# Optimization experiments

Measured on AMD Instinct MI355X. Metric: run time of the kernel, lower is better.

The kernel has to match this reference:

```python
import jax, jax.numpy as jnp
import numpy as np

R, B, F, C, NCLS = 32, 4096, 256, 4, 1000  # n_rules, batch, n_fea, n_channel, n_cls
K, PAD, POOL = 5, 1, 2                     # kernel_size, padding, pooling_size


def setup_inputs() -> dict:
    key = jax.random.key(0)
    ks = jax.random.split(key, 12)
    L0 = F + 2 * PAD - K + 1          # 254 after conv1
    L1 = L0 // POOL                   # 127 after avgpool1
    L2 = (L1 + 2 * PAD - K + 1) // POOL  # 62 after conv2+avgpool2
    att = C * L2                      # 248 (matches torch att_size formula)
    hid = att // 2                    # 124
    s = lambda k, shape: jax.random.normal(k, shape, dtype=jnp.float32) * 0.05
    return dict(
        data=jax.random.normal(ks[0], (B, F), dtype=jnp.float32),
        proto=s(ks[1], (R, F)),
        conv1_w=s(ks[2], (C, 1, K)), conv1_b=s(ks[3], (C,)),
        conv2_w=s(ks[4], (C, C, K)), conv2_b=s(ks[5], (C,)),
        fc1_w=s(ks[6], (att, hid)), fc1_b=s(ks[7], (hid,)),
        fc2_w=s(ks[8], (hid, 1)), fc2_b=s(ks[9], (1,)),
        consq_w=s(ks[10], (R, F, NCLS)), consq_b=s(ks[11], (R, NCLS)),
        is_train=0,
    )


def _conv1d(x, w, b):
    # x: [N, Cin, L], w: [Cout, Cin, K]
    out = jax.lax.conv_general_dilated(
        x, w, window_strides=(1,), padding=[(PAD, PAD)],
        dimension_numbers=('NCH', 'OIH', 'NCH'))
    return out + b[None, :, None]


def _avgpool2(x):
    # non-overlapping AvgPool1d(2), drops trailing remainder like torch
    L2 = x.shape[-1] // POOL
    return x[..., :L2 * POOL].reshape(x.shape[0], x.shape[1], L2, POOL).mean(-1)


def reference(data, proto, conv1_w, conv1_b, conv2_w, conv2_b,
              fc1_w, fc1_b, fc2_w, fc2_b, consq_w, consq_b, is_train):
    n_batch = data.shape[0]
    # data_diff: [R, B, F] -> shared gating net, fold rules into batch
    diff = (data[None, :, :] - proto[:, None, :]).reshape(R * n_batch, 1, F)
    h = _avgpool2(jax.nn.relu(_conv1d(diff, conv1_w, conv1_b)))
    h = _avgpool2(jax.nn.relu(_conv1d(h, conv2_w, conv2_b)))
    h = h.reshape(R * n_batch, -1)                       # [R*B, att]
    h = jax.nn.relu(h @ fc1_w + fc1_b)                   # [R*B, hid]
    fs_ini = jnp.tanh(h @ fc2_w + fc2_b)                 # [R*B, 1]
    fs_ini = fs_ini.reshape(R, n_batch).T                # cat(dim=1) -> [B, R]
    fs = jax.nn.softmax(fs_ini, axis=1)                  # softmax over rules
    # per-rule experts: grouped matmul [B,F] x [R,F,NCLS]
    expert = jnp.einsum('bf,rfc->rbc', data, consq_w) + consq_b[:, None, :]
    return jnp.einsum('br,rbc->bc', fs, expert)          # [B, NCLS]
```

## Files before the change

kernel.cpp:

```cpp
#include <hip/hip_runtime.h>
#include <hip/hip_bf16.h>

using bf16x8 = __attribute__((ext_vector_type(8))) short;
using f32x4  = __attribute__((ext_vector_type(4))) float;
using v2f    = __attribute__((ext_vector_type(2))) float;

__device__ __forceinline__ unsigned short f2bf_rne(float x) {
    unsigned u = __float_as_uint(x);
    u += 0x7fffu + ((u >> 16) & 1u);
    return (unsigned short)(u >> 16);
}

__device__ __forceinline__ float sload(float v) {
    return __uint_as_float(__builtin_amdgcn_readfirstlane(__float_as_uint(v)));
}

__device__ __forceinline__ void gload_lds16(const void* g, void* l) {
    __builtin_amdgcn_global_load_lds(
        (const __attribute__((address_space(1))) unsigned int*)g,
        (__attribute__((address_space(3))) unsigned int*)l, 16, 0, 0);
}

constexpr int KP = 8320;
constexpr int KROW = KP * 2;

constexpr size_t OFF_DT  = 0;
constexpr size_t OFF_Q1  = OFF_DT  + (size_t)260 * 4096 * 4;
constexpr size_t OFF_BT  = OFF_Q1  + (size_t)32 * 1024 * 4;
constexpr size_t OFF_C1P = OFF_BT;
constexpr size_t OFF_W1S = OFF_BT  + (size_t)1024 * KP * 2;
constexpr size_t OFF_FSI = OFF_W1S + (size_t)128 * 256 * 2;
constexpr size_t OFF_FS  = OFF_FSI + (size_t)32 * 4096 * 4;
constexpr size_t OFF_ASC = OFF_FS  + (size_t)32 * 4096 * 4;
constexpr size_t OFF_H2  = OFF_ASC;
constexpr size_t OFF_P1  = OFF_ASC + (size_t)4096 * KP * 2;

__global__ __launch_bounds__(256) void k_transpose(const float* __restrict__ data,
                                                   float* __restrict__ dTp) {
    __shared__ float tile[64][65];
    int bx = blockIdx.x & 63;
    int fx = blockIdx.x >> 6;
    int tx = threadIdx.x & 63, ty4 = threadIdx.x >> 6;
#pragma unroll
    for (int i = 0; i < 16; ++i) {
        int ty = ty4 * 16 + i;
        tile[ty][tx] = data[(bx * 64 + ty) * 256 + fx * 64 + tx];
    }
    __syncthreads();
#pragma unroll
    for (int i = 0; i < 16; ++i) {
        int ty = ty4 * 16 + i;
        dTp[(size_t)(fx * 64 + ty + 1) * 4096 + bx * 64 + tx] = tile[tx][ty];
    }
}

__global__ __launch_bounds__(256) void k_zrows(float* __restrict__ dTp) {
    int i = blockIdx.x * 256 + threadIdx.x;
    dTp[i] = 0.f;
    dTp[(size_t)257 * 4096 + i] = 0.f;
}

__global__ __launch_bounds__(256) void k_prep_proto(const float* __restrict__ proto,
                                                    const float* __restrict__ w1,
                                                    const float* __restrict__ b1,
                                                    float* __restrict__ q1p) {
    __shared__ float ps[256];
    __shared__ float w1s[20];
    int r = blockIdx.x, tid = threadIdx.x;
    ps[tid] = proto[r * 256 + tid];
    if (tid < 20) w1s[tid] = w1[tid];
    __syncthreads();
    if (tid < 254) {
#pragma unroll
        for (int c = 0; c < 4; ++c) {
            float s = -b1[c];
#pragma unroll
            for (int k = 0; k < 5; ++k) {
                int x = tid + k - 1;
                float xv = (x >= 0 && x < 256) ? ps[x] : 0.f;
                s += w1s[c * 5 + k] * xv;
            }
            q1p[r * 1024 + c * 256 + tid] = s;
        }
    }
}

__global__ __launch_bounds__(64) void k_prep_c1d(const float* __restrict__ dTp,
                                                 const float* __restrict__ w1,
                                                 float2* __restrict__ c1p) {
    int lane = threadIdx.x;
    int bg = blockIdx.x >> 3, ch = blockIdx.x & 7;
    int l0 = ch << 4;
    int nl = (ch == 7) ? 15 : 16;
    int b = (bg << 6) + lane;
    float w1r[20];
#pragma unroll
    for (int i = 0; i < 20; ++i) w1r[i] = w1[i];
    const float* dp = dTp + (size_t)(2 * l0) * 4096 + b;
    float d[6];
#pragma unroll
    for (int i = 0; i < 6; ++i) d[i] = dp[(size_t)i * 4096];
    dp += (size_t)6 * 4096;
    float2* outp = c1p + b;
    for (int li = 0; li < nl; ++li) {
        int l = l0 + li;
#pragma unroll
        for (int c = 0; c < 4; ++c) {
            float s0 = 0.f, s1 = 0.f;
#pragma unroll
            for (int k = 0; k < 5; ++k) {
                s0 += w1r[c * 5 + k] * d[k];
                s1 += w1r[c * 5 + k] * d[k + 1];
            }
            outp[(size_t)(c * 127 + l) * 4096] = make_float2(s0, s1);
        }
        d[0] = d[2]; d[1] = d[3]; d[2] = d[4]; d[3] = d[5];
        d[4] = dp[0];
        d[5] = dp[4096];
        dp += 8192;
    }
}

__global__ __launch_bounds__(256) void k_castB(const float* __restrict__ cw,
                                               const float* __restrict__ cb,
                                               unsigned short* __restrict__ BT) {
    __shared__ unsigned short L[64 * 137];
    int tid = threadIdx.x;
    int kt = blockIdx.x >> 3, ct = blockIdx.x & 7;
    int k0 = kt << 6, c0 = ct << 7;
#pragma unroll
    for (int i = 0; i < 32; ++i) {
        int flat = i * 256 + tid;
        int cl = flat & 127, kl = flat >> 7;
        int cg = c0 + cl;
        int kg = k0 + kl;
        float v = 0.f;
        if (cg < 1000) {
            if (kg < 8192) v = cw[(size_t)kg * 1000 + cg];
            else if (kg < 8224) v = cb[(size_t)(kg - 8192) * 1000 + cg];
        }
        L[kl * 137 + cl] = f2bf_rne(v);
    }
    __syncthreads();
#pragma unroll
    for (int i = 0; i < 4; ++i) {
        int task = i * 256 + tid;
        int kg = task & 7, cl = task >> 3;
        int base = kg * 8 * 137 + cl;
        unsigned x = (unsigned)L[base] | ((unsigned)L[base + 137] << 16);
        unsigned y = (unsigned)L[base + 2 * 137] | ((unsigned)L[base + 3 * 137] << 16);
        unsigned z = (unsigned)L[base + 4 * 137] | ((unsigned)L[base + 5 * 137] << 16);
        unsigned w = (unsigned)L[base + 6 * 137] | ((unsigned)L[base + 7 * 137] << 16);
        uint4 o; o.x = x; o.y = y; o.z = z; o.w = w;
        int cg = c0 + cl;
        size_t byte = (size_t)cg * KROW + (size_t)(kt << 7) + (size_t)((kg ^ (cg & 7)) << 4);
        *(uint4*)((char*)BT + byte) = o;
    }
}

__global__ __launch_bounds__(256) void k_castW(const float* __restrict__ fc1w,
                                               unsigned short* __restrict__ W1s) {
    int idx = blockIdx.x * 256 + threadIdx.x;
    int col = idx >> 8, k = idx & 255;
    float v = 0.f;
    if (col < 124 && k < 248) {
        int f = (k & 3) * 62 + (k >> 2);
        v = fc1w[f * 124 + col];
    }
    int byte = col * 512 + ((k >> 6) << 7) + ((((k >> 3) & 7) ^ (col & 7)) << 4) + ((k & 7) << 1);
    *(unsigned short*)((char*)W1s + byte) = f2bf_rne(v);
}

__global__ __attribute__((amdgpu_waves_per_eu(3, 4))) __launch_bounds__(64)
void k_conv2(const float2* __restrict__ c1p,
             const float* __restrict__ q1p,
             const float* __restrict__ w2,
             const float* __restrict__ b2,
             char* __restrict__ h2c) {
    __shared__ unsigned short T[64 * 72];

    int lane = threadIdx.x;
    int job = blockIdx.x;
    int jh = job & 1;
    int bc = (job >> 1) & 63;
    int r  = job >> 7;
    int b0 = bc << 6;
    int b = b0 + lane;
    int rb0 = r * 4096 + b0;
    int j2s = jh ? 32 : 0;
    int j2e = jh ? 62 : 32;

    float w2r[80];
#pragma unroll
    for (int i = 0; i < 80; ++i) w2r[i] = sload(w2[i]);
    v2f bb[4];
#pragma unroll
    for (int c = 0; c < 4; ++c) { float t = sload(b2[c]); bb[c][0] = t; bb[c][1] = t; }

    const float* q1row = q1p + r * 1024;

    auto pooled = [&](int c, int l) -> float {
        float2 v = c1p[(size_t)(c * 127 + l) * 4096 + b];
        float2 q = *(const float2*)(q1row + c * 256 + 2 * l);
        return 0.5f * (fmaxf(v.x - q.x, 0.f) + fmaxf(v.y - q.y, 0.f));
    };

    v2f P[4][5];
#pragma unroll
    for (int c = 0; c < 4; ++c) {
        float pv[6];
#pragma unroll
        for (int idx = 0; idx < 6; ++idx) {
            int l = 2 * j2s - 1 + idx;
            pv[idx] = (l < 0) ? 0.f : pooled(c, l);
        }
#pragma unroll
        for (int k = 0; k < 5; ++k) { P[c][k][0] = pv[k]; P[c][k][1] = pv[k + 1]; }
    }

#pragma unroll 2
    for (int j2 = j2s; j2 < j2e; ++j2) {
        v2f u[4];
#pragma unroll
        for (int c = 0; c < 4; ++c) u[c] = bb[c];
#pragma unroll
        for (int c = 0; c < 4; ++c)
#pragma unroll
            for (int ci = 0; ci < 4; ++ci)
#pragma unroll
                for (int k = 0; k < 5; ++k)
                    u[c] += P[ci][k] * w2r[(c * 4 + ci) * 5 + k];
        {
            float h0 = 0.5f * (fmaxf(u[0][0], 0.f) + fmaxf(u[0][1], 0.f));
            float h1 = 0.5f * (fmaxf(u[1][0], 0.f) + fmaxf(u[1][1], 0.f));
            float h2v = 0.5f * (fmaxf(u[2][0], 0.f) + fmaxf(u[2][1], 0.f));
            float h3 = 0.5f * (fmaxf(u[3][0], 0.f) + fmaxf(u[3][1], 0.f));
            uint2 vv;
            vv.x = (unsigned)f2bf_rne(h0) | ((unsigned)f2bf_rne(h1) << 16);
            vv.y = (unsigned)f2bf_rne(h2v) | ((unsigned)f2bf_rne(h3) << 16);
            *(uint2*)(T + lane * 72 + (j2 & 15) * 4) = vv;
        }
        if (j2 == 61) {
            uint4 z; z.x = z.y = z.z = z.w = 0u;
            *(uint4*)(T + lane * 72 + 56) = z;
        }
        if ((j2 & 15) == 15 || j2 == 61) {
            int chunk = j2 >> 4;
            int g = lane & 7;
#pragma unroll
            for (int i = 0; i < 8; ++i) {
                int sL = i * 8 + (lane >> 3);
                bf16x8 v = *(const bf16x8*)(T + sL * 72 + g * 8);
                int srow = rb0 + sL;
                size_t byte = (size_t)srow * 512 + (size_t)(chunk * 128) + (size_t)((g ^ (srow & 7)) << 4);
                *(bf16x8*)(h2c + byte) = v;
            }
        }
        if (j2 < j2e - 1) {
#pragma unroll
            for (int c = 0; c < 4; ++c) {
                float n0 = pooled(c, 2 * j2 + 5);
                float n1 = pooled(c, 2 * j2 + 6);
                v2f p4v = P[c][4];
                P[c][0] = P[c][2]; P[c][1] = P[c][3]; P[c][2] = p4v;
                v2f t3; t3[0] = p4v[1]; t3[1] = n0;
                v2f t4; t4[0] = n0;     t4[1] = n1;
                P[c][3] = t3; P[c][4] = t4;
            }
        }
    }
}

__global__ __launch_bounds__(256) void k_fc(const char* __restrict__ h2,
                                            const char* __restrict__ W1s,
                                            const float* __restrict__ fc1b,
                                            const float* __restrict__ fc2w,
                                            const float* __restrict__ fc2b,
                                            float* __restrict__ fsiniT) {
    int tid = threadIdx.x, lane = tid & 63, w = tid >> 6;
    int row0 = blockIdx.x * 128 + w * 32;
    int lr = lane & 15, g = lane >> 4, rxor = lr & 7;

    f32x4 acc[2][8] = {};

    const char* arow0 = h2 + (size_t)(row0 + lr) * 512;
    const char* arow1 = arow0 + 16 * 512;

    auto inrowf = [&](int ks) {
        return ((ks >> 1) << 7) + ((((ks * 4 + g) & 7) ^ rxor) << 4);
    };

    bf16x8 a0 = *(const bf16x8*)(arow0 + inrowf(0));
    bf16x8 a1 = *(const bf16x8*)(arow1 + inrowf(0));

#pragma unroll
    for (int ks = 0; ks < 8; ++ks) {
        int ir = inrowf(ks);
        bf16x8 bfr[8];
#pragma unroll
        for (int nf = 0; nf < 8; ++nf)
            bfr[nf] = *(const bf16x8*)(W1s + (nf * 16 + lr) * 512 + ir);
        bf16x8 an0 = a0, an1 = a1;
        if (ks < 7) {
            int ir2 = inrowf(ks + 1);
            an0 = *(const bf16x8*)(arow0 + ir2);
            an1 = *(const bf16x8*)(arow1 + ir2);
        }
#pragma unroll
        for (int nf = 0; nf < 8; ++nf) {
            acc[0][nf] = __builtin_amdgcn_mfma_f32_16x16x32_bf16(a0, bfr[nf], acc[0][nf], 0, 0, 0);
            acc[1][nf] = __builtin_amdgcn_mfma_f32_16x16x32_bf16(a1, bfr[nf], acc[1][nf], 0, 0, 0);
        }
        a0 = an0; a1 = an1;
    }

    float zp[2][4] = {};
#pragma unroll
    for (int nf = 0; nf < 8; ++nf) {
        int col = nf * 16 + lr;
        float b1v = (col < 124) ? fc1b[col] : 0.f;
        float w2v = (col < 124) ? fc2w[col] : 0.f;
#pragma unroll
        for (int mf = 0; mf < 2; ++mf)
#pragma unroll
            for (int q = 0; q < 4; ++q) {
                float h = fmaxf(acc[mf][nf][q] + b1v, 0.f);
                zp[mf][q] += h * w2v;
            }
    }
#pragma unroll
    for (int off = 1; off < 16; off <<= 1) {
#pragma unroll
        for (int mf = 0; mf < 2; ++mf)
#pragma unroll
            for (int q = 0; q < 4; ++q)
                zp[mf][q] += __shfl_xor(zp[mf][q], off, 64);
    }
    if (lr == 0) {
        float c2 = fc2b[0];
#pragma unroll
        for (int mf = 0; mf < 2; ++mf)
#pragma unroll
            for (int q = 0; q < 4; ++q) {
                int srow = row0 + mf * 16 + g * 4 + q;
                fsiniT[srow] = tanhf(zp[mf][q] + c2);
            }
    }
}

__global__ __launch_bounds__(256) void k_softmax(const float* __restrict__ fsiniT,
                                                 float* __restrict__ fsT) {
    int b = blockIdx.x * 256 + threadIdx.x;
    float v[32];
    float m = -1e30f;
#pragma unroll
    for (int r = 0; r < 32; ++r) { v[r] = fsiniT[r * 4096 + b]; m = fmaxf(m, v[r]); }
    float s = 0.f;
#pragma unroll
    for (int r = 0; r < 32; ++r) { v[r] = expf(v[r] - m); s += v[r]; }
    float inv = 1.f / s;
#pragma unroll
    for (int r = 0; r < 32; ++r) fsT[r * 4096 + b] = v[r] * inv;
}

__global__ __launch_bounds__(256) void k_scaleA(const float* __restrict__ data,
                                                const float* __restrict__ fsT,
                                                unsigned short* __restrict__ Asc) {
    int g = blockIdx.x * 256 + threadIdx.x;
    int b = g / 1040, kg = g - b * 1040;
    uint4 o;
    unsigned* op = (unsigned*)&o;
    if (kg < 1024) {
        int r = kg >> 5, f0 = (kg & 31) << 3;
        float fs = fsT[r * 4096 + b];
        const float4* dp = (const float4*)(data + b * 256 + f0);
        float4 v0 = dp[0], v1 = dp[1];
        float vals[8] = {v0.x, v0.y, v0.z, v0.w, v1.x, v1.y, v1.z, v1.w};
#pragma unroll
        for (int i = 0; i < 4; ++i) {
            unsigned lo = f2bf_rne(vals[2 * i] * fs);
            unsigned hi = f2bf_rne(vals[2 * i + 1] * fs);
            op[i] = lo | (hi << 16);
        }
    } else {
        int base = (kg - 1024) << 3;
        op[0] = op[1] = op[2] = op[3] = 0u;
        if (base < 32) {
#pragma unroll
            for (int i = 0; i < 4; ++i) {
                unsigned lo = f2bf_rne(fsT[(base + 2 * i) * 4096 + b]);
                unsigned hi = f2bf_rne(fsT[(base + 2 * i + 1) * 4096 + b]);
                op[i] = lo | (hi << 16);
            }
        }
    }
    size_t byte = (size_t)b * KROW + (size_t)((kg & ~7) << 4) + (size_t)(((kg & 7) ^ (b & 7)) << 4);
    *(uint4*)((char*)Asc + byte) = o;
}

__global__ __launch_bounds__(512) void k_gemm(const unsigned short* __restrict__ Asc,
                                              const unsigned short* __restrict__ BT,
                                              float* __restrict__ out,
                                              _Float16* __restrict__ part1) {
    __shared__ unsigned short As[2][8192];
    __shared__ unsigned short Bs[2][8192];
    int tid = threadIdx.x, lane = tid & 63, w = tid >> 6;
    int wm = w >> 2, wn = w & 3;
    int bid = blockIdx.x;
    int xcd = bid & 7, idx = bid >> 3;
    int mt = (xcd << 2) | (idx >> 4);
    int nt = (idx >> 1) & 7;
    int ks = idx & 1;
    int row0 = mt << 7, col0 = nt << 7;

    f32x4 acc[4][2] = {};

    const char* Ab = (const char*)Asc + (size_t)ks * (KP);
    const char* Bb = (const char*)BT + (size_t)ks * (KP);
    int flat0 = tid * 16, flat1 = tid * 16 + 8192;
    int rowl0 = flat0 >> 7, colB0 = flat0 & 127;
    int rowl1 = flat1 >> 7, colB1 = flat1 & 127;
    const char* aSrc0 = Ab + (size_t)(row0 + rowl0) * KROW + colB0;
    const char* aSrc1 = Ab + (size_t)(row0 + rowl1) * KROW + colB1;
    const char* bSrc0 = Bb + (size_t)(col0 + rowl0) * KROW + colB0;
    const char* bSrc1 = Bb + (size_t)(col0 + rowl1) * KROW + colB1;

    auto stage = [&](int buf, int kt) {
        int off = kt << 7;
        gload_lds16(aSrc0 + off, (char*)&As[buf][0] + flat0);
        gload_lds16(aSrc1 + off, (char*)&As[buf][0] + flat1);
        gload_lds16(bSrc0 + off, (char*)&Bs[buf][0] + flat0);
        gload_lds16(bSrc1 + off, (char*)&Bs[buf][0] + flat1);
    };

    auto compute = [&](int buf) {
        const char* Asb = (const char*)&As[buf][0];
        const char* Bsb = (const char*)&Bs[buf][0];
#pragma unroll
        for (int s = 0; s < 2; ++s) {
            bf16x8 af[4], bfv[2];
            int colByte = ((s << 5) + ((lane >> 4) << 3)) << 1;
#pragma unroll
            for (int mi = 0; mi < 4; ++mi) {
                int rowA = (wm << 6) + (mi << 4) + (lane & 15);
                int byte = (rowA << 7) + colByte;
                af[mi] = *(const bf16x8*)(Asb + (byte ^ ((rowA & 7) << 4)));
            }
#pragma unroll
            for (int ni = 0; ni < 2; ++ni) {
                int rowB = (wn << 5) + (ni << 4) + (lane & 15);
                int byte = (rowB << 7) + colByte;
                bfv[ni] = *(const bf16x8*)(Bsb + (byte ^ ((rowB & 7) << 4)));
            }
#pragma unroll
            for (int mi = 0; mi < 4; ++mi)
#pragma unroll
                for (int ni = 0; ni < 2; ++ni)
                    acc[mi][ni] = __builtin_amdgcn_mfma_f32_16x16x32_bf16(af[mi], bfv[ni], acc[mi][ni], 0, 0, 0);
        }
    };

    stage(0, 0);
    asm volatile("s_waitcnt vmcnt(0)" ::: "memory");
    __syncthreads();
#pragma unroll 1
    for (int kt = 0; kt < 64; ++kt) {
        stage((kt + 1) & 1, kt + 1);
        compute(kt & 1);
        asm volatile("s_waitcnt vmcnt(0)" ::: "memory");
        __syncthreads();
    }
    compute(0);

    int cA = col0 + (wn << 5) + (lane & 15);
    int cB2 = cA + 16;
    int rbase = row0 + (wm << 6) + ((lane >> 4) << 2);

    if (ks == 0) {
#pragma unroll
        for (int mi = 0; mi < 4; ++mi)
#pragma unroll
            for (int q = 0; q < 4; ++q) {
                int row = rbase + mi * 16 + q;
                if (cA < 1000) out[row * 1000 + cA] = acc[mi][0][q];
                if (cB2 < 1000) out[row * 1000 + cB2] = acc[mi][1][q];
            }
    } else {
#pragma unroll
        for (int mi = 0; mi < 4; ++mi)
#pragma unroll
            for (int q = 0; q < 4; ++q) {
                int row = rbase + mi * 16 + q;
                if (cA < 1000) part1[row * 1000 + cA] = (_Float16)acc[mi][0][q];
                if (cB2 < 1000) part1[row * 1000 + cB2] = (_Float16)acc[mi][1][q];
            }
    }
}

__global__ __launch_bounds__(256) void k_reduce(float* __restrict__ out,
                                                const _Float16* __restrict__ p1) {
    int i = (blockIdx.x * 256 + threadIdx.x) * 4;
    float4 o = *(float4*)(out + i);
    o.x += (float)p1[i];
    o.y += (float)p1[i + 1];
    o.z += (float)p1[i + 2];
    o.w += (float)p1[i + 3];
    *(float4*)(out + i) = o;
}

extern "C" void kernel_launch(void* const* d_in, const int* in_sizes, int n_in,
                              void* d_out, int out_size, void* d_ws, size_t ws_size,
                              hipStream_t stream) {
    const float* data  = (const float*)d_in[0];
    const float* proto = (const float*)d_in[1];
    const float* w1    = (const float*)d_in[2];
    const float* b1    = (const float*)d_in[3];
    const float* w2    = (const float*)d_in[4];
    const float* b2    = (const float*)d_in[5];
    const float* fc1w  = (const float*)d_in[6];
    const float* fc1b  = (const float*)d_in[7];
    const float* fc2w  = (const float*)d_in[8];
    const float* fc2b  = (const float*)d_in[9];
    const float* cw    = (const float*)d_in[10];
    const float* cbias = (const float*)d_in[11];
    float* out = (float*)d_out;
    char* ws = (char*)d_ws;

    float* dTp             = (float*)(ws + OFF_DT);
    float* q1p             = (float*)(ws + OFF_Q1);
    float2* c1p            = (float2*)(ws + OFF_C1P);
    unsigned short* BT     = (unsigned short*)(ws + OFF_BT);
    unsigned short* W1s    = (unsigned short*)(ws + OFF_W1S);
    float* fsiniT          = (float*)(ws + OFF_FSI);
    float* fsT             = (float*)(ws + OFF_FS);
    unsigned short* Asc    = (unsigned short*)(ws + OFF_ASC);
    char* h2c              = (char*)(ws + OFF_H2);
    _Float16* part1        = (_Float16*)(ws + OFF_P1);

    hipLaunchKernelGGL(k_transpose, dim3(256), dim3(256), 0, stream, data, dTp);
    hipLaunchKernelGGL(k_zrows, dim3(16), dim3(256), 0, stream, dTp);
    hipLaunchKernelGGL(k_prep_proto, dim3(32), dim3(256), 0, stream, proto, w1, b1, q1p);
    hipLaunchKernelGGL(k_prep_c1d, dim3(512), dim3(64), 0, stream, dTp, w1, c1p);
    hipLaunchKernelGGL(k_conv2, dim3(4096), dim3(64), 0, stream, c1p, q1p, w2, b2, h2c);
    hipLaunchKernelGGL(k_castB, dim3(1040), dim3(256), 0, stream, cw, cbias, BT);
    hipLaunchKernelGGL(k_castW, dim3(128), dim3(256), 0, stream, fc1w, W1s);
    hipLaunchKernelGGL(k_fc, dim3(1024), dim3(256), 0, stream,
                       h2c, (const char*)W1s, fc1b, fc2w, fc2b, fsiniT);
    hipLaunchKernelGGL(k_softmax, dim3(16), dim3(256), 0, stream, fsiniT, fsT);
    hipLaunchKernelGGL(k_scaleA, dim3(16640), dim3(256), 0, stream, data, fsT, Asc);
    hipLaunchKernelGGL(k_gemm, dim3(512), dim3(512), 0, stream, Asc, BT, out, part1);
    hipLaunchKernelGGL(k_reduce, dim3(4000), dim3(256), 0, stream, out, part1);
}
```

Before: 261.4 us.

## Compute conv2 with bf16 MFMA over LDS-staged pooled activations

Rewrites the conv2 stage so each block loads the pooled conv1 activations for 32 samples into LDS as bf16. It then runs conv2 as a 16x16x32 bf16 MFMA against a banded weight fragment, with output positions and taps folded into the K dimension, and pools adjacent outputs through a lane shuffle. This replaces the per-lane scalar FMA loop, which held 80 weights in registers, and moves work from VALU onto matrix cores. The costs are bf16 rounding of the conv2 inputs and weights, larger LDS use, and two block-wide barriers.

```diff
diff --git a/kernel.cpp b/kernel.cpp
--- a/kernel.cpp
+++ b/kernel.cpp
@@ -9,10 +9,6 @@
     unsigned u = __float_as_uint(x);
     u += 0x7fffu + ((u >> 16) & 1u);
     return (unsigned short)(u >> 16);
-}
-
-__device__ __forceinline__ float sload(float v) {
-    return __uint_as_float(__builtin_amdgcn_readfirstlane(__float_as_uint(v)));
 }
 
 __device__ __forceinline__ void gload_lds16(const void* g, void* l) {
@@ -171,103 +167,95 @@
     *(unsigned short*)((char*)W1s + byte) = f2bf_rne(v);
 }
 
-__global__ __attribute__((amdgpu_waves_per_eu(3, 4))) __launch_bounds__(64)
-void k_conv2(const float2* __restrict__ c1p,
-             const float* __restrict__ q1p,
-             const float* __restrict__ w2,
-             const float* __restrict__ b2,
-             char* __restrict__ h2c) {
-    __shared__ unsigned short T[64 * 72];
-
-    int lane = threadIdx.x;
+__global__ __launch_bounds__(128) void k_conv2(const float2* __restrict__ c1p,
+                                               const float* __restrict__ q1p,
+                                               const float* __restrict__ w2,
+                                               const float* __restrict__ b2,
+                                               char* __restrict__ h2c) {
+    __shared__ unsigned short P1[32 * 536];
+    __shared__ unsigned short T2[256 * 36];
+
+    int tid = threadIdx.x;
+    int w = tid >> 6, lane = tid & 63;
     int job = blockIdx.x;
-    int jh = job & 1;
-    int bc = (job >> 1) & 63;
-    int r  = job >> 7;
-    int b0 = bc << 6;
-    int b = b0 + lane;
+    int r = job >> 7;
+    int b0 = (job & 127) << 5;
     int rb0 = r * 4096 + b0;
-    int j2s = jh ? 32 : 0;
-    int j2e = jh ? 62 : 32;
-
-    float w2r[80];
-#pragma unroll
-    for (int i = 0; i < 80; ++i) w2r[i] = sload(w2[i]);
-    v2f bb[4];
-#pragma unroll
-    for (int c = 0; c < 4; ++c) { float t = sload(b2[c]); bb[c][0] = t; bb[c][1] = t; }
-
-    const float* q1row = q1p + r * 1024;
-
-    auto pooled = [&](int c, int l) -> float {
-        float2 v = c1p[(size_t)(c * 127 + l) * 4096 + b];
-        float2 q = *(const float2*)(q1row + c * 256 + 2 * l);
-        return 0.5f * (fmaxf(v.x - q.x, 0.f) + fmaxf(v.y - q.y, 0.f));
-    };
-
-    v2f P[4][5];
-#pragma unroll
-    for (int c = 0; c < 4; ++c) {
-        float pv[6];
-#pragma unroll
-        for (int idx = 0; idx < 6; ++idx) {
-            int l = 2 * j2s - 1 + idx;
-            pv[idx] = (l < 0) ? 0.f : pooled(c, l);
-        }
-#pragma unroll
-        for (int k = 0; k < 5; ++k) { P[c][k][0] = pv[k]; P[c][k][1] = pv[k + 1]; }
-    }
-
-#pragma unroll 2
-    for (int j2 = j2s; j2 < j2e; ++j2) {
-        v2f u[4];
-#pragma unroll
-        for (int c = 0; c < 4; ++c) u[c] = bb[c];
-#pragma unroll
-        for (int c = 0; c < 4; ++c)
-#pragma unroll
-            for (int ci = 0; ci < 4; ++ci)
-#pragma unroll
-                for (int k = 0; k < 5; ++k)
-                    u[c] += P[ci][k] * w2r[(c * 4 + ci) * 5 + k];
-        {
-            float h0 = 0.5f * (fmaxf(u[0][0], 0.f) + fmaxf(u[0][1], 0.f));
-            float h1 = 0.5f * (fmaxf(u[1][0], 0.f) + fmaxf(u[1][1], 0.f));
-            float h2v = 0.5f * (fmaxf(u[2][0], 0.f) + fmaxf(u[2][1], 0.f));
-            float h3 = 0.5f * (fmaxf(u[3][0], 0.f) + fmaxf(u[3][1], 0.f));
-            uint2 vv;
-            vv.x = (unsigned)f2bf_rne(h0) | ((unsigned)f2bf_rne(h1) << 16);
-            vv.y = (unsigned)f2bf_rne(h2v) | ((unsigned)f2bf_rne(h3) << 16);
-            *(uint2*)(T + lane * 72 + (j2 & 15) * 4) = vv;
-        }
-        if (j2 == 61) {
-            uint4 z; z.x = z.y = z.z = z.w = 0u;
-            *(uint4*)(T + lane * 72 + 56) = z;
-        }
-        if ((j2 & 15) == 15 || j2 == 61) {
-            int chunk = j2 >> 4;
-            int g = lane & 7;
-#pragma unroll
-            for (int i = 0; i < 8; ++i) {
-                int sL = i * 8 + (lane >> 3);
-                bf16x8 v = *(const bf16x8*)(T + sL * 72 + g * 8);
-                int srow = rb0 + sL;
-                size_t byte = (size_t)srow * 512 + (size_t)(chunk * 128) + (size_t)((g ^ (srow & 7)) << 4);
-                *(bf16x8*)(h2c + byte) = v;
-            }
-        }
-        if (j2 < j2e - 1) {
-#pragma unroll
-            for (int c = 0; c < 4; ++c) {
-                float n0 = pooled(c, 2 * j2 + 5);
-                float n1 = pooled(c, 2 * j2 + 6);
-                v2f p4v = P[c][4];
-                P[c][0] = P[c][2]; P[c][1] = P[c][3]; P[c][2] = p4v;
-                v2f t3; t3[0] = p4v[1]; t3[1] = n0;
-                v2f t4; t4[0] = n0;     t4[1] = n1;
-                P[c][3] = t3; P[c][4] = t4;
-            }
-        }
+
+    int n = lane & 15, g = lane >> 4;
+    int cc = n & 3, tt = (n >> 2) & 1, dj = n >> 3;
+    short tmpB[8] __attribute__((aligned(16)));
+#pragma unroll
+    for (int e = 0; e < 8; ++e) {
+        int k = g * 8 + e;
+        int lof = k >> 2, ci = k & 3;
+        int tap = lof - 2 * dj - tt;
+        float v = (tap >= 0 && tap <= 4) ? w2[(cc * 4 + ci) * 5 + tap] : 0.f;
+        tmpB[e] = (short)f2bf_rne(v);
+    }
+    bf16x8 Bfrag = *(bf16x8*)tmpB;
+    float bc = b2[cc];
+
+    if (tid < 32) *(uint2*)(&P1[tid * 536]) = make_uint2(0u, 0u);
+    for (int i = tid; i < 8 * 36; i += 128) T2[248 * 36 + i] = 0;
+
+    {
+        int cl = lane >> 5;
+        int s  = lane & 31;
+        int l_beg = w ? 64 : 0;
+        int l_end = w ? 127 : 64;
+        const float* q1row = q1p + r * 1024;
+        for (int l = l_beg; l < l_end; ++l) {
+#pragma unroll
+            for (int c2 = 0; c2 < 2; ++c2) {
+                int c = c2 * 2 + cl;
+                float2 v = c1p[(size_t)(c * 127 + l) * 4096 + b0 + s];
+                float2 q = *(const float2*)(q1row + c * 256 + 2 * l);
+                float pv = 0.5f * (fmaxf(v.x - q.x, 0.f) + fmaxf(v.y - q.y, 0.f));
+                P1[s * 536 + (l + 1) * 4 + c] = f2bf_rne(pv);
+            }
+        }
+    }
+    __syncthreads();
+
+    {
+        int p_beg = w ? 16 : 0;
+        int p_end = w ? 31 : 16;
+        for (int p = p_beg; p < p_end; ++p) {
+#pragma unroll
+            for (int mt = 0; mt < 2; ++mt) {
+                int s = mt * 16 + n;
+                bf16x8 Af = *(const bf16x8*)((const char*)P1 + s * 1072 + 32 * p + g * 16);
+                f32x4 acc = {};
+                acc = __builtin_amdgcn_mfma_f32_16x16x32_bf16(Af, Bfrag, acc, 0, 0, 0);
+                f32x4 part;
+#pragma unroll
+                for (int q_ = 0; q_ < 4; ++q_) part[q_] = __shfl_xor(acc[q_], 4, 64);
+                if (!(lane & 4)) {
+                    int j2 = 2 * p + dj;
+                    int k = j2 * 4 + cc;
+                    unsigned short hh[4] __attribute__((aligned(8)));
+#pragma unroll
+                    for (int q_ = 0; q_ < 4; ++q_) {
+                        float h = 0.5f * (fmaxf(acc[q_] + bc, 0.f) + fmaxf(part[q_] + bc, 0.f));
+                        hh[q_] = f2bf_rne(h);
+                    }
+                    *(uint2*)(&T2[k * 36 + mt * 16 + g * 4]) = *(uint2*)hh;
+                }
+            }
+        }
+    }
+    __syncthreads();
+
+    for (int u = tid; u < 1024; u += 128) {
+        int s = u & 31, k8 = u >> 5;
+        unsigned short v8[8] __attribute__((aligned(16)));
+#pragma unroll
+        for (int e = 0; e < 8; ++e) v8[e] = T2[(k8 * 8 + e) * 36 + s];
+        int srow = rb0 + s;
+        size_t byte = (size_t)srow * 512 + (size_t)((k8 >> 3) << 7)
+                    + (size_t)(((k8 & 7) ^ (srow & 7)) << 4);
+        *(bf16x8*)(h2c + byte) = *(bf16x8*)v8;
     }
 }
 
@@ -541,7 +529,7 @@
     hipLaunchKernelGGL(k_zrows, dim3(16), dim3(256), 0, stream, dTp);
     hipLaunchKernelGGL(k_prep_proto, dim3(32), dim3(256), 0, stream, proto, w1, b1, q1p);
     hipLaunchKernelGGL(k_prep_c1d, dim3(512), dim3(64), 0, stream, dTp, w1, c1p);
-    hipLaunchKernelGGL(k_conv2, dim3(4096), dim3(64), 0, stream, c1p, q1p, w2, b2, h2c);
+    hipLaunchKernelGGL(k_conv2, dim3(4096), dim3(128), 0, stream, c1p, q1p, w2, b2, h2c);
     hipLaunchKernelGGL(k_castB, dim3(1040), dim3(256), 0, stream, cw, cbias, BT);
     hipLaunchKernelGGL(k_castW, dim3(128), dim3(256), 0, stream, fc1w, W1s);
     hipLaunchKernelGGL(k_fc, dim3(1024), dim3(256), 0, stream,
```

New measurement: 285.2 us. 1.09x slower.
